# Kernel tuning notes

Measured on AMD Instinct MI355X. Metric: run time of the kernel, lower is better.

Reference implementation:

```python
import jax, jax.numpy as jnp
import numpy as np

T, B, DICO, EMB, LAT = 256, 64, 8192, 256, 256


def setup_inputs() -> dict:
    key = jax.random.key(0)
    ks = jax.random.split(key, 7)
    s_emb = 1.0 / np.sqrt(DICO)
    s_enc = 1.0 / np.sqrt(EMB + LAT)
    return {
        "x": jax.random.normal(ks[0], (T, B, DICO), dtype=jnp.float32),
        "h": jax.random.normal(ks[1], (B, LAT), dtype=jnp.float32),
        "W_emb": jax.random.uniform(ks[2], (DICO, EMB), jnp.float32, -s_emb, s_emb),
        "b_emb": jax.random.uniform(ks[3], (EMB,), jnp.float32, -s_emb, s_emb),
        "W_enc": jax.random.uniform(ks[4], (EMB + LAT, LAT), jnp.float32, -s_enc, s_enc),
        "b_enc": jax.random.uniform(ks[5], (LAT,), jnp.float32, -s_enc, s_enc),
    }


def reference(x, h, W_emb, b_emb, W_enc, b_enc):
    # embedding: [T,B,DICO] @ [DICO,EMB] -> [T,B,EMB]
    xe = jnp.einsum('tbd,de->tbe', x, W_emb) + b_emb
    # split encoder weight into x-part and h-part: cat(x,h)@W == x@Wx + h@Wh
    Wx, Wh = W_enc[:EMB], W_enc[EMB:]
    # hoist the per-step x projection out of the scan (no h dependence)
    xp = jnp.einsum('tbe,el->tbl', xe, Wx) + b_enc  # [T,B,LAT]

    def step(h, xp_t):
        h_new = jnp.tanh(xp_t + h @ Wh)
        return h_new, h_new

    _, hs = jax.lax.scan(step, h, xp)
    return hs  # [T,B,LAT]
```

## Files before the change

kernel.cpp:

```cpp
#include <hip/hip_runtime.h>
#include <hip/hip_bf16.h>
#include <stdint.h>

#define T_DIM 256
#define B_DIM 64
#define DICO  8192
#define EMB   256
#define LAT   256
#define M_DIM (T_DIM*B_DIM)

#define BM 128
#define BN 256
#define BK 64
#define KSPLIT 2
#define KCHUNK (DICO/KSPLIT)
#define NKS (KCHUNK/BK)

typedef short  bf16x8 __attribute__((ext_vector_type(8)));
typedef float  f32x4  __attribute__((ext_vector_type(4)));
typedef _Float16 f16x2 __attribute__((ext_vector_type(2)));

__device__ __forceinline__ ushort f2bf(float f) {
  uint32_t u = __float_as_uint(f);
  u += 0x7FFFu + ((u >> 16) & 1u);
  return (ushort)(u >> 16);
}

__device__ __forceinline__ void glds16(const void* g, void* l) {
  __builtin_amdgcn_global_load_lds(
      (const __attribute__((address_space(1))) uint32_t*)g,
      (__attribute__((address_space(3))) uint32_t*)l, 16, 0, 0);
}

__global__ void wct_kernel(const float* __restrict__ Wemb, const float* __restrict__ Wenc,
                           ushort* __restrict__ wct) {
  const int n  = threadIdx.x;
  const int d0 = blockIdx.x * 32;
  __shared__ float we[32 * 256];
  __shared__ float tr[32 * 257];
  #pragma unroll
  for (int r = 0; r < 32; ++r) we[r*256 + n] = Wemb[(size_t)(d0 + r)*EMB + n];
  __syncthreads();
  float acc[32];
  #pragma unroll
  for (int d = 0; d < 32; ++d) acc[d] = 0.f;
  #pragma unroll 4
  for (int e = 0; e < 256; ++e) {
    float wv = Wenc[e*LAT + n];
    #pragma unroll
    for (int d = 0; d < 32; ++d) acc[d] += we[d*256 + e] * wv;
  }
  #pragma unroll
  for (int d = 0; d < 32; ++d) tr[d*257 + n] = acc[d];
  __syncthreads();
  const int nn0 = n >> 2, kc = n & 3;
  #pragma unroll
  for (int p = 0; p < 4; ++p) {
    int nn = p*64 + nn0;
    bf16x8 v;
    #pragma unroll
    for (int j = 0; j < 8; ++j) v[j] = (short)f2bf(tr[(kc*8 + j)*257 + nn]);
    *(bf16x8*)(wct + (size_t)nn*DICO + d0 + kc*8) = v;
  }
}

__global__ void __launch_bounds__(512, 1) gemm_kernel(const float* __restrict__ x,
                                                      const ushort* __restrict__ wct,
                                                      float* __restrict__ xp) {
  __shared__ __align__(16) ushort sA[2][BM * BK];
  __shared__ __align__(16) ushort sB[2][BN * BK];
  const int tid = threadIdx.x;
  const int bid = blockIdx.x;
  const int swzb = (bid & 7) * 32 + (bid >> 3);
  const int mt = swzb & 127, ksp = swzb >> 7;
  const size_t rowbase = (size_t)mt * BM;
  const int kbase = ksp * KCHUNK;

  const int lane = tid & 63, wid = tid >> 6;
  const int l15 = lane & 15, lc = lane >> 4;
  const int wr = wid >> 2, wc = wid & 3;

  const int r0 = tid >> 2, c0 = tid & 3;
  const float* ag = x + (rowbase + r0) * (size_t)DICO + kbase + c0 * 16;
  const int sx0 = (((2*c0    ) ^ (r0 & 7)) * 16);
  const int sx1 = (((2*c0 + 1) ^ (r0 & 7)) * 16);

  const int sw0 = (((    lc) ^ (l15 & 7)) * 16);
  const int sw1 = (((4 + lc) ^ (l15 & 7)) * 16);

  const char* wb = (const char*)wct;
  const size_t kb2 = (size_t)kbase * 2;

  const int brow_s = (tid >> 3);
  const int bslot_s = tid & 7;

  f32x4 acc[4][4];
  #pragma unroll
  for (int m = 0; m < 4; ++m)
    #pragma unroll
    for (int n = 0; n < 4; ++n) acc[m][n] = (f32x4){0.f, 0.f, 0.f, 0.f};

  float4 av[4];

  auto loadA = [&](int kofs) {
    #pragma unroll
    for (int q = 0; q < 4; ++q) av[q] = *(const float4*)(ag + kofs + q * 4);
  };
  auto stageB = [&](int buf, int kofs) {
    #pragma unroll
    for (int r = 0; r < 4; ++r) {
      const int row = r * 64 + brow_s;
      const int srcslot = bslot_s ^ (row & 7);
      glds16(wb + (size_t)row * (DICO * 2) + kb2 + (size_t)kofs * 2 + srcslot * 16,
             (char*)&sB[buf][0] + r * 8192 + tid * 16);
    }
  };
  auto storeA = [&](int buf) {
    const float4 a0 = av[0], a1 = av[1], a2 = av[2], a3 = av[3];
    bf16x8 w0, w1;
    w0[0]=(short)f2bf(a0.x); w0[1]=(short)f2bf(a0.y); w0[2]=(short)f2bf(a0.z); w0[3]=(short)f2bf(a0.w);
    w0[4]=(short)f2bf(a1.x); w0[5]=(short)f2bf(a1.y); w0[6]=(short)f2bf(a1.z); w0[7]=(short)f2bf(a1.w);
    w1[0]=(short)f2bf(a2.x); w1[1]=(short)f2bf(a2.y); w1[2]=(short)f2bf(a2.z); w1[3]=(short)f2bf(a2.w);
    w1[4]=(short)f2bf(a3.x); w1[5]=(short)f2bf(a3.y); w1[6]=(short)f2bf(a3.z); w1[7]=(short)f2bf(a3.w);
    char* base = (char*)&sA[buf][0] + r0 * 128;
    *(bf16x8*)(base + sx0) = w0;
    *(bf16x8*)(base + sx1) = w1;
  };
  auto compute = [&](int buf) {
    bf16x8 bfr[4][2];
    #pragma unroll
    for (int n = 0; n < 4; ++n) {
      const char* bb = (const char*)&sB[buf][0] + (wc*64 + n*16 + l15) * 128;
      bfr[n][0] = *(const bf16x8*)(bb + sw0);
      bfr[n][1] = *(const bf16x8*)(bb + sw1);
    }
    #pragma unroll
    for (int m = 0; m < 4; ++m) {
      const char* ab = (const char*)&sA[buf][0] + (wr*64 + m*16 + l15) * 128;
      bf16x8 a0 = *(const bf16x8*)(ab + sw0);
      bf16x8 a1 = *(const bf16x8*)(ab + sw1);
      #pragma unroll
      for (int n = 0; n < 4; ++n) {
        acc[m][n] = __builtin_amdgcn_mfma_f32_16x16x32_bf16(a0, bfr[n][0], acc[m][n], 0, 0, 0);
        acc[m][n] = __builtin_amdgcn_mfma_f32_16x16x32_bf16(a1, bfr[n][1], acc[m][n], 0, 0, 0);
      }
    }
  };

  loadA(0);
  stageB(0, 0);
  storeA(0);
  __syncthreads();

  int cur = 0;
  for (int ks = 0; ks < NKS; ++ks) {
    const int kn = (ks + 1) * BK;
    if (ks + 1 < NKS) { loadA(kn); stageB(cur ^ 1, kn); }
    compute(cur);
    if (ks + 1 < NKS) storeA(cur ^ 1);
    __syncthreads();
    cur ^= 1;
  }

  float* xpo = xp + ((size_t)ksp * M_DIM + rowbase) * LAT;
  #pragma unroll
  for (int m = 0; m < 4; ++m)
    #pragma unroll
    for (int n = 0; n < 4; ++n)
      #pragma unroll
      for (int j = 0; j < 4; ++j)
        xpo[(size_t)(wr*64 + m*16 + lc*4 + j) * LAT + wc*64 + n*16 + l15] = acc[m][n][j];
}

__global__ void __launch_bounds__(256, 1) rnn_kernel(const float* __restrict__ xp,
                           const float* __restrict__ h0, const float* __restrict__ Wenc,
                           const float* __restrict__ bemb, const float* __restrict__ benc,
                           float* __restrict__ out) {
  const int b = blockIdx.x, l = threadIdx.x;
  __shared__ __align__(16) uint32_t hbuf[2][128];
  float bc = benc[l];
  #pragma unroll 8
  for (int e = 0; e < 256; ++e) bc += bemb[e] * Wenc[e*LAT + l];
  f16x2 wh[128];
  #pragma unroll
  for (int j = 0; j < 128; ++j) {
    f16x2 w;
    w[0] = (_Float16)Wenc[(size_t)(EMB + 2*j    )*LAT + l];
    w[1] = (_Float16)Wenc[(size_t)(EMB + 2*j + 1)*LAT + l];
    wh[j] = w;
  }
  ((_Float16*)&hbuf[0][0])[l] = (_Float16)h0[(size_t)b*LAT + l];
  __syncthreads();
  const float* xpb = xp + (size_t)b*LAT + l;
  float*       ob  = out + (size_t)b*LAT + l;
  const size_t ST = (size_t)B_DIM * LAT;
  const size_t PO = (size_t)M_DIM * LAT;
  float xa0 = xpb[0],  xa1 = xpb[PO];
  float xb0 = xpb[ST], xb1 = xpb[ST + PO];
  float xc0 = 0.f, xc1 = 0.f;
  for (int t = 0; t < T_DIM; ++t) {
    if (t + 2 < T_DIM) {
      size_t ni = (size_t)(t + 2) * ST;
      xc0 = xpb[ni]; xc1 = xpb[ni + PO];
    }
    const uint32_t* hc = &hbuf[t & 1][0];
    float s0=0.f,s1=0.f,s2=0.f,s3=0.f,s4=0.f,s5=0.f,s6=0.f,s7=0.f;
    #pragma unroll
    for (int q = 0; q < 16; ++q) {
      uint4 hv0 = *(const uint4*)(hc + q*8);
      uint4 hv1 = *(const uint4*)(hc + q*8 + 4);
      s0 = __builtin_amdgcn_fdot2(wh[q*8+0], __builtin_bit_cast(f16x2, hv0.x), s0, false);
      s1 = __builtin_amdgcn_fdot2(wh[q*8+1], __builtin_bit_cast(f16x2, hv0.y), s1, false);
      s2 = __builtin_amdgcn_fdot2(wh[q*8+2], __builtin_bit_cast(f16x2, hv0.z), s2, false);
      s3 = __builtin_amdgcn_fdot2(wh[q*8+3], __builtin_bit_cast(f16x2, hv0.w), s3, false);
      s4 = __builtin_amdgcn_fdot2(wh[q*8+4], __builtin_bit_cast(f16x2, hv1.x), s4, false);
      s5 = __builtin_amdgcn_fdot2(wh[q*8+5], __builtin_bit_cast(f16x2, hv1.y), s5, false);
      s6 = __builtin_amdgcn_fdot2(wh[q*8+6], __builtin_bit_cast(f16x2, hv1.z), s6, false);
      s7 = __builtin_amdgcn_fdot2(wh[q*8+7], __builtin_bit_cast(f16x2, hv1.w), s7, false);
    }
    float pre = (xa0 + xa1) + bc + (((s0+s1)+(s2+s3)) + ((s4+s5)+(s6+s7)));
    float ax = fabsf(pre);
    float e2 = __expf(-2.f * ax);
    float r  = __fdividef(1.f - e2, 1.f + e2);
    float hn = (pre < 0.f) ? -r : r;
    ob[(size_t)t * ST] = hn;
    ((_Float16*)&hbuf[(t + 1) & 1][0])[l] = (_Float16)hn;
    __builtin_amdgcn_sched_barrier(0);
    asm volatile("s_waitcnt lgkmcnt(0)" ::: "memory");
    __builtin_amdgcn_s_barrier();
    __builtin_amdgcn_sched_barrier(0);
    xa0 = xb0; xa1 = xb1; xb0 = xc0; xb1 = xc1;
  }
}

extern "C" void kernel_launch(void* const* d_in, const int* in_sizes, int n_in,
                              void* d_out, int out_size, void* d_ws, size_t ws_size,
                              hipStream_t stream) {
  const float* x    = (const float*)d_in[0];
  const float* h0   = (const float*)d_in[1];
  const float* Wemb = (const float*)d_in[2];
  const float* bemb = (const float*)d_in[3];
  const float* Wenc = (const float*)d_in[4];
  const float* benc = (const float*)d_in[5];
  float* out = (float*)d_out;

  ushort* wct = (ushort*)d_ws;
  float*  xp  = (float*)((char*)d_ws + ((size_t)4 << 20));

  wct_kernel<<<256, 256, 0, stream>>>(Wemb, Wenc, wct);
  gemm_kernel<<<256, 512, 0, stream>>>(x, wct, xp);
  rnn_kernel<<<64, 256, 0, stream>>>(xp, h0, Wenc, bemb, benc, out);
}
```

Measured before the change: 673.2 us.

## Halve GEMM M-tile, single-buffer LDS, run two 256-thread blocks per CU

Shrinks the GEMM block tile from 128 to 64 rows and launches 512 blocks of 256 threads instead of 256 blocks of 512, with launch bounds allowing two blocks per CU. Shared memory drops from double to single buffering, so the main loop now syncs twice per K step: it stores A and stages B, syncs, then prefetches the next A chunk into registers and computes. The aim is more resident waves and a finer grid to hide the latency of the memory-bound x read. In exchange it loses the LDS double-buffer overlap and adds a barrier per step.

```diff
diff --git a/kernel.cpp b/kernel.cpp
--- a/kernel.cpp
+++ b/kernel.cpp
@@ -9,7 +9,7 @@
 #define LAT   256
 #define M_DIM (T_DIM*B_DIM)
 
-#define BM 128
+#define BM 64
 #define BN 256
 #define BK 64
 #define KSPLIT 2
@@ -64,21 +64,20 @@
   }
 }
 
-__global__ void __launch_bounds__(512, 1) gemm_kernel(const float* __restrict__ x,
+__global__ void __launch_bounds__(256, 2) gemm_kernel(const float* __restrict__ x,
                                                       const ushort* __restrict__ wct,
                                                       float* __restrict__ xp) {
-  __shared__ __align__(16) ushort sA[2][BM * BK];
-  __shared__ __align__(16) ushort sB[2][BN * BK];
+  __shared__ __align__(16) ushort sA[BM * BK];
+  __shared__ __align__(16) ushort sB[BN * BK];
   const int tid = threadIdx.x;
   const int bid = blockIdx.x;
-  const int swzb = (bid & 7) * 32 + (bid >> 3);
-  const int mt = swzb & 127, ksp = swzb >> 7;
+  const int swzb = (bid & 7) * 64 + (bid >> 3);
+  const int mt = swzb & 255, ksp = swzb >> 8;
   const size_t rowbase = (size_t)mt * BM;
   const int kbase = ksp * KCHUNK;
 
   const int lane = tid & 63, wid = tid >> 6;
   const int l15 = lane & 15, lc = lane >> 4;
-  const int wr = wid >> 2, wc = wid & 3;
 
   const int r0 = tid >> 2, c0 = tid & 3;
   const float* ag = x + (rowbase + r0) * (size_t)DICO + kbase + c0 * 16;
@@ -106,37 +105,37 @@
     #pragma unroll
     for (int q = 0; q < 4; ++q) av[q] = *(const float4*)(ag + kofs + q * 4);
   };
-  auto stageB = [&](int buf, int kofs) {
-    #pragma unroll
-    for (int r = 0; r < 4; ++r) {
-      const int row = r * 64 + brow_s;
+  auto stageB = [&](int kofs) {
+    #pragma unroll
+    for (int r = 0; r < 8; ++r) {
+      const int row = r * 32 + brow_s;
       const int srcslot = bslot_s ^ (row & 7);
       glds16(wb + (size_t)row * (DICO * 2) + kb2 + (size_t)kofs * 2 + srcslot * 16,
-             (char*)&sB[buf][0] + r * 8192 + tid * 16);
-    }
-  };
-  auto storeA = [&](int buf) {
+             (char*)sB + r * 4096 + tid * 16);
+    }
+  };
+  auto storeA = [&]() {
     const float4 a0 = av[0], a1 = av[1], a2 = av[2], a3 = av[3];
     bf16x8 w0, w1;
     w0[0]=(short)f2bf(a0.x); w0[1]=(short)f2bf(a0.y); w0[2]=(short)f2bf(a0.z); w0[3]=(short)f2bf(a0.w);
     w0[4]=(short)f2bf(a1.x); w0[5]=(short)f2bf(a1.y); w0[6]=(short)f2bf(a1.z); w0[7]=(short)f2bf(a1.w);
     w1[0]=(short)f2bf(a2.x); w1[1]=(short)f2bf(a2.y); w1[2]=(short)f2bf(a2.z); w1[3]=(short)f2bf(a2.w);
     w1[4]=(short)f2bf(a3.x); w1[5]=(short)f2bf(a3.y); w1[6]=(short)f2bf(a3.z); w1[7]=(short)f2bf(a3.w);
-    char* base = (char*)&sA[buf][0] + r0 * 128;
+    char* base = (char*)sA + r0 * 128;
     *(bf16x8*)(base + sx0) = w0;
     *(bf16x8*)(base + sx1) = w1;
   };
-  auto compute = [&](int buf) {
+  auto compute = [&]() {
     bf16x8 bfr[4][2];
     #pragma unroll
     for (int n = 0; n < 4; ++n) {
-      const char* bb = (const char*)&sB[buf][0] + (wc*64 + n*16 + l15) * 128;
+      const char* bb = (const char*)sB + (wid*64 + n*16 + l15) * 128;
       bfr[n][0] = *(const bf16x8*)(bb + sw0);
       bfr[n][1] = *(const bf16x8*)(bb + sw1);
     }
     #pragma unroll
     for (int m = 0; m < 4; ++m) {
-      const char* ab = (const char*)&sA[buf][0] + (wr*64 + m*16 + l15) * 128;
+      const char* ab = (const char*)sA + (m*16 + l15) * 128;
       bf16x8 a0 = *(const bf16x8*)(ab + sw0);
       bf16x8 a1 = *(const bf16x8*)(ab + sw1);
       #pragma unroll
@@ -148,18 +147,13 @@
   };
 
   loadA(0);
-  stageB(0, 0);
-  storeA(0);
-  __syncthreads();
-
-  int cur = 0;
   for (int ks = 0; ks < NKS; ++ks) {
-    const int kn = (ks + 1) * BK;
-    if (ks + 1 < NKS) { loadA(kn); stageB(cur ^ 1, kn); }
-    compute(cur);
-    if (ks + 1 < NKS) storeA(cur ^ 1);
     __syncthreads();
-    cur ^= 1;
+    storeA();
+    stageB(ks * BK);
+    __syncthreads();
+    if (ks + 1 < NKS) loadA((ks + 1) * BK);
+    compute();
   }
 
   float* xpo = xp + ((size_t)ksp * M_DIM + rowbase) * LAT;
@@ -169,7 +163,7 @@
     for (int n = 0; n < 4; ++n)
       #pragma unroll
       for (int j = 0; j < 4; ++j)
-        xpo[(size_t)(wr*64 + m*16 + lc*4 + j) * LAT + wc*64 + n*16 + l15] = acc[m][n][j];
+        xpo[(size_t)(m*16 + lc*4 + j) * LAT + wid*64 + n*16 + l15] = acc[m][n][j];
 }
 
 __global__ void __launch_bounds__(256, 1) rnn_kernel(const float* __restrict__ xp,
@@ -248,6 +242,6 @@
   float*  xp  = (float*)((char*)d_ws + ((size_t)4 << 20));
 
   wct_kernel<<<256, 256, 0, stream>>>(Wemb, Wenc, wct);
-  gemm_kernel<<<256, 512, 0, stream>>>(x, wct, xp);
+  gemm_kernel<<<512, 256, 0, stream>>>(x, wct, xp);
   rnn_kernel<<<64, 256, 0, stream>>>(xp, h0, Wenc, bemb, benc, out);
 }
```

Result: no change. 660.4 us (-1.9%).
